# Optimization experiments

Hardware: AMD Instinct MI355X
Metric: run time of the kernel (lower is better)

Reference implementation:

```python
import jax, jax.numpy as jnp
import numpy as np

D_MODEL = 1024

def setup_inputs() -> dict:
    key = jax.random.key(0)
    ks = jax.random.split(key, 9)
    s = 1.0 / np.sqrt(D_MODEL)
    x = jax.random.normal(ks[0], (4, 2048, D_MODEL), dtype=jnp.float32)
    Wq = jax.random.uniform(ks[1], (D_MODEL, D_MODEL), jnp.float32, -s, s)
    bq = jax.random.uniform(ks[2], (D_MODEL,), jnp.float32, -s, s)
    Wk = jax.random.uniform(ks[3], (D_MODEL, D_MODEL), jnp.float32, -s, s)
    bk = jax.random.uniform(ks[4], (D_MODEL,), jnp.float32, -s, s)
    Wv = jax.random.uniform(ks[5], (D_MODEL, D_MODEL), jnp.float32, -s, s)
    bv = jax.random.uniform(ks[6], (D_MODEL,), jnp.float32, -s, s)
    Wo = jax.random.uniform(ks[7], (D_MODEL, D_MODEL), jnp.float32, -s, s)
    bo = jax.random.uniform(ks[8], (D_MODEL,), jnp.float32, -s, s)
    return {"x": x, "Wq": Wq, "bq": bq, "Wk": Wk, "bk": bk,
            "Wv": Wv, "bv": bv, "Wo": Wo, "bo": bo}

def reference(x, Wq, bq, Wk, bk, Wv, bv, Wo, bo):
    # Linear projections (weights stored as [in, out])
    q = x @ Wq + bq  # [b, s, d]
    k = x @ Wk + bk
    v = x @ Wv + bv
    d_k = q.shape[-1]
    scores = jnp.einsum("bqd,bkd->bqk", q, k) / jnp.sqrt(jnp.float32(d_k))
    p = jax.nn.softmax(scores, axis=-1)
    attn = jnp.einsum("bqk,bkd->bqd", p, v)
    return attn @ Wo + bo
```

## Files before the change

kernel.cpp:

```cpp
#include <hip/hip_runtime.h>
#include <stdint.h>

#define D_MODEL 1024
#define SEQ 2048
#define NBATCH 4

typedef __attribute__((ext_vector_type(4))) float f32x4;
typedef __attribute__((ext_vector_type(8))) __bf16 bf16x8;
typedef __attribute__((ext_vector_type(4))) unsigned short u16x4;

__device__ __forceinline__ float b2f(unsigned short u) {
    union { unsigned int i; float f; } c; c.i = ((unsigned int)u) << 16; return c.f;
}
__device__ __forceinline__ unsigned short f2b(float f) {
    union { float f; unsigned int i; } c; c.f = f;
    unsigned int u = c.i;
    u += 0x7FFFu + ((u >> 16) & 1u);
    return (unsigned short)(u >> 16);
}

__device__ __forceinline__ void glds16(void* lds, const void* g) {
    __builtin_amdgcn_global_load_lds((const __attribute__((address_space(1))) void*)g,
                                     (__attribute__((address_space(3))) void*)lds,
                                     16, 0, 0);
}

__device__ __forceinline__ void cfence() { asm volatile("" ::: "memory"); }

__device__ __forceinline__ void xcd_map(int& xx, int& yy, int& zz)
{
    const int gx = gridDim.x, gy = gridDim.y;
    int bid = blockIdx.x + gx * (blockIdx.y + gy * blockIdx.z);
    const int H = gy >> 3;
    const int xcd = bid & 7;
    int slot = bid >> 3;
    yy = xcd * H + (slot % H);
    slot /= H;
    xx = slot % gx;
    zz = slot / gx;
}

__device__ __forceinline__ void gemm_tile(const unsigned short* __restrict__ A,
                                          const unsigned short* __restrict__ Bt,
                                          int K, int m0, int n0,
                                          f32x4 (&acc)[4][4])
{
    __shared__ alignas(16) unsigned short As[3 * 128 * 32];
    __shared__ alignas(16) unsigned short Bs[3 * 128 * 32];

    const int t    = threadIdx.x;
    const int wave = t >> 6;
    const int lane = t & 63;

    const int srow = (wave << 4) + (lane >> 2);
    const int sch  = ((lane & 3) ^ ((srow >> 1) & 3)) * 8;

    const unsigned short* Ag = A  + (long)(m0 + srow) * K + sch;
    const unsigned short* Bg = Bt + (long)(n0 + srow) * K + sch;

    char* AsW = (char*)As + wave * 1024;
    char* BsW = (char*)Bs + wave * 1024;

    const int fr = lane & 15, quad = lane >> 4;
    const int wm = (wave >> 1) * 64, wn = (wave & 1) * 64;
    const int slot = (quad ^ ((fr >> 1) & 3)) * 16;
    const int aoff = (wm + fr) * 64 + slot;
    const int boff = (wn + fr) * 64 + slot;

    const int nt = K >> 5;

    auto stage = [&](int buf, int ko) {
        #pragma unroll
        for (int j = 0; j < 2; ++j) {
            glds16(AsW + buf * 8192 + j * 4096, Ag + (long)(j * 64) * K + ko);
            glds16(BsW + buf * 8192 + j * 4096, Bg + (long)(j * 64) * K + ko);
        }
    };

    stage(0, 0);
    stage(1, 32);
    asm volatile("s_waitcnt vmcnt(4)" ::: "memory");
    __builtin_amdgcn_sched_barrier(0);
    cfence(); __builtin_amdgcn_s_barrier(); cfence();

    int br = 0, bw = 2, ko = 64;
    for (int ti = 0; ti < nt; ++ti) {
        const char* Ab = (const char*)As + br * 8192;
        const char* Bb = (const char*)Bs + br * 8192;
        bf16x8 af[4], bv[4];
        #pragma unroll
        for (int i = 0; i < 4; ++i)
            af[i] = *(const bf16x8*)(Ab + aoff + i * 1024);
        #pragma unroll
        for (int i = 0; i < 4; ++i)
            bv[i] = *(const bf16x8*)(Bb + boff + i * 1024);

        const bool pf = (ti + 2 < nt);
        if (pf) { stage(bw, ko); ko += 32; }

        __builtin_amdgcn_s_setprio(1);
        #pragma unroll
        for (int mi = 0; mi < 4; ++mi)
            #pragma unroll
            for (int ni = 0; ni < 4; ++ni)
                acc[mi][ni] = __builtin_amdgcn_mfma_f32_16x16x32_bf16(
                                  af[mi], bv[ni], acc[mi][ni], 0, 0, 0);
        __builtin_amdgcn_s_setprio(0);

        if (pf)               asm volatile("s_waitcnt vmcnt(4)" ::: "memory");
        else if (ti + 1 < nt) asm volatile("s_waitcnt vmcnt(0)" ::: "memory");
        __builtin_amdgcn_sched_barrier(0);
        cfence(); __builtin_amdgcn_s_barrier(); cfence();

        br = (br == 2) ? 0 : br + 1;
        bw = (bw == 2) ? 0 : bw + 1;
    }
}

template<bool BIAS, typename OutT>
__global__ __launch_bounds__(256)
void gemm_bt(const unsigned short* __restrict__ A,
             const unsigned short* __restrict__ Bt,
             const float* __restrict__ bias,
             OutT* __restrict__ C,
             int N, int K, long sA, long sB, long sC)
{
    int xx, yy, zz;
    xcd_map(xx, yy, zz);
    A  += (long)zz * sA;
    Bt += (long)zz * sB;
    C  += (long)zz * sC;
    const int m0 = yy * 128;
    const int n0 = xx * 128;

    f32x4 acc[4][4] = {};
    gemm_tile(A, Bt, K, m0, n0, acc);

    const int t = threadIdx.x, wave = t >> 6, lane = t & 63;
    const int wm = (wave >> 1) * 64, wn = (wave & 1) * 64;
    const int fr = lane & 15, quad = lane >> 4;

    float bb[4] = {0.f, 0.f, 0.f, 0.f};
    if (BIAS) {
        #pragma unroll
        for (int ni = 0; ni < 4; ++ni)
            bb[ni] = bias[n0 + wn + ni * 16 + fr];
    }

    #pragma unroll
    for (int mi = 0; mi < 4; ++mi) {
        const int rowb = m0 + wm + mi * 16 + quad * 4;
        #pragma unroll
        for (int ni = 0; ni < 4; ++ni) {
            const int col = n0 + wn + ni * 16 + fr;
            f32x4 v = acc[mi][ni];
            if constexpr (sizeof(OutT) == 4) {
                #pragma unroll
                for (int r = 0; r < 4; ++r)
                    C[(long)(rowb + r) * N + col] = v[r] + bb[ni];
            } else {
                #pragma unroll
                for (int r = 0; r < 4; ++r)
                    C[(long)(rowb + r) * N + col] = (OutT)f2b(v[r] + bb[ni]);
            }
        }
    }
}

__global__ __launch_bounds__(256)
void qkv_gemm(const unsigned short* __restrict__ xb,
              const unsigned short* __restrict__ Wqt,
              const unsigned short* __restrict__ Wkt,
              const unsigned short* __restrict__ Wvt,
              const float* __restrict__ bq, const float* __restrict__ bk,
              const float* __restrict__ bv,
              unsigned short* __restrict__ Q, unsigned short* __restrict__ Kb,
              unsigned short* __restrict__ Vt)
{
    int xx, yy, zz;
    xcd_map(xx, yy, zz);

    const unsigned short* Bt; const float* bias; unsigned short* C; bool tstore = false;
    switch (zz) {
        case 0:  Bt = Wqt; bias = bq; C = Q;  break;
        case 1:  Bt = Wkt; bias = bk; C = Kb; break;
        default: Bt = Wvt; bias = bv; C = Vt; tstore = true; break;
    }
    const int m0 = yy * 128;
    const int n0 = xx * 128;
    const int N = D_MODEL, K = D_MODEL;

    f32x4 acc[4][4] = {};
    gemm_tile(xb, Bt, K, m0, n0, acc);

    const int t = threadIdx.x, wave = t >> 6, lane = t & 63;
    const int wm = (wave >> 1) * 64, wn = (wave & 1) * 64;
    const int fr = lane & 15, quad = lane >> 4;

    float bb[4];
    #pragma unroll
    for (int ni = 0; ni < 4; ++ni)
        bb[ni] = bias[n0 + wn + ni * 16 + fr];

    #pragma unroll
    for (int mi = 0; mi < 4; ++mi) {
        const int rowb = m0 + wm + mi * 16 + quad * 4;
        #pragma unroll
        for (int ni = 0; ni < 4; ++ni) {
            const int col = n0 + wn + ni * 16 + fr;
            f32x4 v = acc[mi][ni];
            if (!tstore) {
                #pragma unroll
                for (int r = 0; r < 4; ++r)
                    C[(long)(rowb + r) * N + col] = f2b(v[r] + bb[ni]);
            } else {
                u16x4 pk;
                #pragma unroll
                for (int r = 0; r < 4; ++r)
                    pk[r] = f2b(v[r] + bb[ni]);
                unsigned short* dst = C + ((long)(rowb >> 11)) * ((long)N * SEQ)
                                        + (long)col * SEQ + (rowb & (SEQ - 1));
                *(u16x4*)dst = pk;
            }
        }
    }
}

__global__ __launch_bounds__(256)
void softmax_inplace(unsigned short* __restrict__ S)
{
    const long row = blockIdx.x;
    unsigned short* s = S + row * SEQ;
    const int t = threadIdx.x;

    u16x4 a = ((const u16x4*)s)[t];
    u16x4 b = ((const u16x4*)s)[t + 256];
    float v[8];
    #pragma unroll
    for (int i = 0; i < 4; ++i) { v[i] = b2f(a[i]); v[4 + i] = b2f(b[i]); }

    float mx = v[0];
    #pragma unroll
    for (int i = 1; i < 8; ++i) mx = fmaxf(mx, v[i]);
    #pragma unroll
    for (int off = 32; off; off >>= 1) mx = fmaxf(mx, __shfl_xor(mx, off));

    __shared__ float red[8];
    const int wv = t >> 6, ln = t & 63;
    if (ln == 0) red[wv] = mx;
    __syncthreads();
    mx = fmaxf(fmaxf(red[0], red[1]), fmaxf(red[2], red[3]));

    const float sc = 0.03125f;
    float e[8], sum = 0.f;
    #pragma unroll
    for (int i = 0; i < 8; ++i) { e[i] = __expf((v[i] - mx) * sc); sum += e[i]; }
    #pragma unroll
    for (int off = 32; off; off >>= 1) sum += __shfl_xor(sum, off);
    if (ln == 0) red[4 + wv] = sum;
    __syncthreads();
    sum = (red[4] + red[5]) + (red[6] + red[7]);
    const float inv = 1.f / sum;

    u16x4 o;
    #pragma unroll
    for (int i = 0; i < 4; ++i) o[i] = f2b(e[i] * inv);
    ((u16x4*)s)[t] = o;
    #pragma unroll
    for (int i = 0; i < 4; ++i) o[i] = f2b(e[4 + i] * inv);
    ((u16x4*)s)[t + 256] = o;
}

__global__ __launch_bounds__(256)
void prep(const float* __restrict__ x, unsigned short* __restrict__ xb,
          const float* __restrict__ W0, const float* __restrict__ W1,
          const float* __restrict__ W2, const float* __restrict__ W3,
          unsigned short* __restrict__ T0, unsigned short* __restrict__ T1,
          unsigned short* __restrict__ T2, unsigned short* __restrict__ T3)
{
    const int bid = blockIdx.x;
    if (bid < 8192) {
        long i = ((long)bid * 256 + threadIdx.x) * 4;
        f32x4 v = *(const f32x4*)(x + i);
        u16x4 o;
        #pragma unroll
        for (int r = 0; r < 4; ++r) o[r] = f2b(v[r]);
        *(u16x4*)(xb + i) = o;
        return;
    }
    const int b2 = bid - 8192;
    const float* W; unsigned short* T;
    switch (b2 >> 10) {
        case 0:  W = W0; T = T0; break;
        case 1:  W = W1; T = T1; break;
        case 2:  W = W2; T = T2; break;
        default: W = W3; T = T3; break;
    }
    const int tile = b2 & 1023;
    const int bx = (tile & 31) * 32, by = (tile >> 5) * 32;
    __shared__ float buf[32][33];
    const int tx = threadIdx.x & 31, ty = threadIdx.x >> 5;
    #pragma unroll
    for (int i = 0; i < 32; i += 8)
        buf[ty + i][tx] = W[(long)(by + ty + i) * D_MODEL + bx + tx];
    __syncthreads();
    #pragma unroll
    for (int i = 0; i < 32; i += 8)
        T[(long)(bx + ty + i) * D_MODEL + by + tx] = f2b(buf[tx][ty + i]);
}

extern "C" void kernel_launch(void* const* d_in, const int* in_sizes, int n_in,
                              void* d_out, int out_size, void* d_ws, size_t ws_size,
                              hipStream_t stream)
{
    const float* x  = (const float*)d_in[0];
    const float* Wq = (const float*)d_in[1];
    const float* bq = (const float*)d_in[2];
    const float* Wk = (const float*)d_in[3];
    const float* bk = (const float*)d_in[4];
    const float* Wv = (const float*)d_in[5];
    const float* bv = (const float*)d_in[6];
    const float* Wo = (const float*)d_in[7];
    const float* bo = (const float*)d_in[8];
    float* out = (float*)d_out;

    char* ws = (char*)d_ws;
    const size_t MB = 1024ull * 1024ull;
    unsigned short* Wqt = (unsigned short*)(ws + 0 * MB);
    unsigned short* Wkt = (unsigned short*)(ws + 2 * MB);
    unsigned short* Wvt = (unsigned short*)(ws + 4 * MB);
    unsigned short* Wot = (unsigned short*)(ws + 6 * MB);
    unsigned short* xb  = (unsigned short*)(ws + 8 * MB);
    unsigned short* Q   = (unsigned short*)(ws + 24 * MB);
    unsigned short* Kb  = (unsigned short*)(ws + 40 * MB);
    unsigned short* Vt  = (unsigned short*)(ws + 56 * MB);
    unsigned short* At  = (unsigned short*)(ws + 72 * MB);
    unsigned short* S   = (unsigned short*)(ws + 88 * MB);

    const dim3 blk(256);

    prep<<<dim3(12288), blk, 0, stream>>>(x, xb, Wq, Wk, Wv, Wo, Wqt, Wkt, Wvt, Wot);

    qkv_gemm<<<dim3(8, 64, 3), blk, 0, stream>>>(xb, Wqt, Wkt, Wvt, bq, bk, bv, Q, Kb, Vt);

    gemm_bt<false, unsigned short><<<dim3(16, 16, 4), blk, 0, stream>>>(
        Q, Kb, nullptr, S, 2048, 1024,
        (long)2048 * 1024, (long)2048 * 1024, (long)2048 * 2048);

    softmax_inplace<<<dim3(NBATCH * SEQ), blk, 0, stream>>>(S);

    gemm_bt<false, unsigned short><<<dim3(8, 16, 4), blk, 0, stream>>>(
        S, Vt, nullptr, At, 1024, 2048,
        (long)2048 * 2048, (long)1024 * 2048, (long)2048 * 1024);

    gemm_bt<true, float><<<dim3(8, 64, 1), blk, 0, stream>>>(
        At, Wot, bo, out, 1024, 1024, 0, 0, 0);
}
```

Baseline: 294.6 us.

## Enlarge GEMM block tile to 256x128 with eight waves per block

All GEMM kernels move from 128x128 tiles with 4 waves to 256x128 tiles with 8 waves (512 threads). Each wave still computes a 64x64 sub-tile. The A staging now issues two row-halves per k-step and B one, with the LDS buffers and vmcnt waits resized to match. Grid sizes are halved along M. This doubles reuse of each loaded B tile and cuts total global traffic. In exchange there are fewer blocks: the PV and output GEMMs drop to 256 blocks, and LDS use per block grows to 72KB, which may hurt latency hiding.

New measurement: 278.2 us. -5.6%, faster.

```diff
diff --git a/kernel.cpp b/kernel.cpp
--- a/kernel.cpp
+++ b/kernel.cpp
@@ -45,7 +45,7 @@
                                           int K, int m0, int n0,
                                           f32x4 (&acc)[4][4])
 {
-    __shared__ alignas(16) unsigned short As[3 * 128 * 32];
+    __shared__ alignas(16) unsigned short As[3 * 256 * 32];
     __shared__ alignas(16) unsigned short Bs[3 * 128 * 32];
 
     const int t    = threadIdx.x;
@@ -62,30 +62,28 @@
     char* BsW = (char*)Bs + wave * 1024;
 
     const int fr = lane & 15, quad = lane >> 4;
-    const int wm = (wave >> 1) * 64, wn = (wave & 1) * 64;
+    const int wr = wave >> 1, wc = wave & 1;
     const int slot = (quad ^ ((fr >> 1) & 3)) * 16;
-    const int aoff = (wm + fr) * 64 + slot;
-    const int boff = (wn + fr) * 64 + slot;
+    const int aoff = (wr * 64 + fr) * 64 + slot;
+    const int boff = (wc * 64 + fr) * 64 + slot;
 
     const int nt = K >> 5;
 
     auto stage = [&](int buf, int ko) {
-        #pragma unroll
-        for (int j = 0; j < 2; ++j) {
-            glds16(AsW + buf * 8192 + j * 4096, Ag + (long)(j * 64) * K + ko);
-            glds16(BsW + buf * 8192 + j * 4096, Bg + (long)(j * 64) * K + ko);
-        }
+        glds16(AsW + buf * 16384,        Ag + ko);
+        glds16(AsW + buf * 16384 + 8192, Ag + (long)128 * K + ko);
+        glds16(BsW + buf * 8192,         Bg + ko);
     };
 
     stage(0, 0);
     stage(1, 32);
-    asm volatile("s_waitcnt vmcnt(4)" ::: "memory");
+    asm volatile("s_waitcnt vmcnt(3)" ::: "memory");
     __builtin_amdgcn_sched_barrier(0);
     cfence(); __builtin_amdgcn_s_barrier(); cfence();
 
     int br = 0, bw = 2, ko = 64;
     for (int ti = 0; ti < nt; ++ti) {
-        const char* Ab = (const char*)As + br * 8192;
+        const char* Ab = (const char*)As + br * 16384;
         const char* Bb = (const char*)Bs + br * 8192;
         bf16x8 af[4], bv[4];
         #pragma unroll
@@ -107,7 +105,7 @@
                                   af[mi], bv[ni], acc[mi][ni], 0, 0, 0);
         __builtin_amdgcn_s_setprio(0);
 
-        if (pf)               asm volatile("s_waitcnt vmcnt(4)" ::: "memory");
+        if (pf)               asm volatile("s_waitcnt vmcnt(3)" ::: "memory");
         else if (ti + 1 < nt) asm volatile("s_waitcnt vmcnt(0)" ::: "memory");
         __builtin_amdgcn_sched_barrier(0);
         cfence(); __builtin_amdgcn_s_barrier(); cfence();
@@ -118,7 +116,7 @@
 }
 
 template<bool BIAS, typename OutT>
-__global__ __launch_bounds__(256)
+__global__ __launch_bounds__(512)
 void gemm_bt(const unsigned short* __restrict__ A,
              const unsigned short* __restrict__ Bt,
              const float* __restrict__ bias,
@@ -130,29 +128,29 @@
     A  += (long)zz * sA;
     Bt += (long)zz * sB;
     C  += (long)zz * sC;
-    const int m0 = yy * 128;
+    const int m0 = yy * 256;
     const int n0 = xx * 128;
 
     f32x4 acc[4][4] = {};
     gemm_tile(A, Bt, K, m0, n0, acc);
 
     const int t = threadIdx.x, wave = t >> 6, lane = t & 63;
-    const int wm = (wave >> 1) * 64, wn = (wave & 1) * 64;
+    const int wr = wave >> 1, wc = wave & 1;
     const int fr = lane & 15, quad = lane >> 4;
 
     float bb[4] = {0.f, 0.f, 0.f, 0.f};
     if (BIAS) {
         #pragma unroll
         for (int ni = 0; ni < 4; ++ni)
-            bb[ni] = bias[n0 + wn + ni * 16 + fr];
+            bb[ni] = bias[n0 + wc * 64 + ni * 16 + fr];
     }
 
     #pragma unroll
     for (int mi = 0; mi < 4; ++mi) {
-        const int rowb = m0 + wm + mi * 16 + quad * 4;
+        const int rowb = m0 + wr * 64 + mi * 16 + quad * 4;
         #pragma unroll
         for (int ni = 0; ni < 4; ++ni) {
-            const int col = n0 + wn + ni * 16 + fr;
+            const int col = n0 + wc * 64 + ni * 16 + fr;
             f32x4 v = acc[mi][ni];
             if constexpr (sizeof(OutT) == 4) {
                 #pragma unroll
@@ -167,7 +165,7 @@
     }
 }
 
-__global__ __launch_bounds__(256)
+__global__ __launch_bounds__(512)
 void qkv_gemm(const unsigned short* __restrict__ xb,
               const unsigned short* __restrict__ Wqt,
               const unsigned short* __restrict__ Wkt,
@@ -186,7 +184,7 @@
         case 1:  Bt = Wkt; bias = bk; C = Kb; break;
         default: Bt = Wvt; bias = bv; C = Vt; tstore = true; break;
     }
-    const int m0 = yy * 128;
+    const int m0 = yy * 256;
     const int n0 = xx * 128;
     const int N = D_MODEL, K = D_MODEL;
 
@@ -194,20 +192,20 @@
     gemm_tile(xb, Bt, K, m0, n0, acc);
 
     const int t = threadIdx.x, wave = t >> 6, lane = t & 63;
-    const int wm = (wave >> 1) * 64, wn = (wave & 1) * 64;
+    const int wr = wave >> 1, wc = wave & 1;
     const int fr = lane & 15, quad = lane >> 4;
 
     float bb[4];
     #pragma unroll
     for (int ni = 0; ni < 4; ++ni)
-        bb[ni] = bias[n0 + wn + ni * 16 + fr];
+        bb[ni] = bias[n0 + wc * 64 + ni * 16 + fr];
 
     #pragma unroll
     for (int mi = 0; mi < 4; ++mi) {
-        const int rowb = m0 + wm + mi * 16 + quad * 4;
+        const int rowb = m0 + wr * 64 + mi * 16 + quad * 4;
         #pragma unroll
         for (int ni = 0; ni < 4; ++ni) {
-            const int col = n0 + wn + ni * 16 + fr;
+            const int col = n0 + wc * 64 + ni * 16 + fr;
             f32x4 v = acc[mi][ni];
             if (!tstore) {
                 #pragma unroll
@@ -337,22 +335,23 @@
     unsigned short* At  = (unsigned short*)(ws + 72 * MB);
     unsigned short* S   = (unsigned short*)(ws + 88 * MB);
 
-    const dim3 blk(256);
-
-    prep<<<dim3(12288), blk, 0, stream>>>(x, xb, Wq, Wk, Wv, Wo, Wqt, Wkt, Wvt, Wot);
-
-    qkv_gemm<<<dim3(8, 64, 3), blk, 0, stream>>>(xb, Wqt, Wkt, Wvt, bq, bk, bv, Q, Kb, Vt);
-
-    gemm_bt<false, unsigned short><<<dim3(16, 16, 4), blk, 0, stream>>>(
+    const dim3 blk256(256);
+    const dim3 blk512(512);
+
+    prep<<<dim3(12288), blk256, 0, stream>>>(x, xb, Wq, Wk, Wv, Wo, Wqt, Wkt, Wvt, Wot);
+
+    qkv_gemm<<<dim3(8, 32, 3), blk512, 0, stream>>>(xb, Wqt, Wkt, Wvt, bq, bk, bv, Q, Kb, Vt);
+
+    gemm_bt<false, unsigned short><<<dim3(16, 8, 4), blk512, 0, stream>>>(
         Q, Kb, nullptr, S, 2048, 1024,
         (long)2048 * 1024, (long)2048 * 1024, (long)2048 * 2048);
 
-    softmax_inplace<<<dim3(NBATCH * SEQ), blk, 0, stream>>>(S);
-
-    gemm_bt<false, unsigned short><<<dim3(8, 16, 4), blk, 0, stream>>>(
+    softmax_inplace<<<dim3(NBATCH * SEQ), blk256, 0, stream>>>(S);
+
+    gemm_bt<false, unsigned short><<<dim3(8, 8, 4), blk512, 0, stream>>>(
         S, Vt, nullptr, At, 1024, 2048,
         (long)2048 * 2048, (long)1024 * 2048, (long)2048 * 1024);
 
-    gemm_bt<true, float><<<dim3(8, 64, 1), blk, 0, stream>>>(
+    gemm_bt<true, float><<<dim3(8, 32, 1), blk512, 0, stream>>>(
         At, Wot, bo, out, 1024, 1024, 0, 0, 0);
 }
```

## Widen GEMM tiles to 128x256 with eight N-fragments per wave

Applied to the files above, without the earlier changes.

Doubles the N dimension of every GEMM block tile from 128 to 256, so each wave computes a 64x128 sub-tile with 32 accumulators instead of 16. B staging loads four 64-row slabs per K-step into a larger LDS buffer, and the grids are halved along x. This raises arithmetic intensity per LDS and global load, but it doubles accumulator register pressure (launch bounds now ask for 2 blocks per CU) and halves the number of blocks. Fewer blocks could underfill the CUs on the smaller launches, such as the 256-block attention-value GEMM.

New measurement: 296.0 us. No clear change (+0.5%).

```diff
diff --git a/kernel.cpp b/kernel.cpp
--- a/kernel.cpp
+++ b/kernel.cpp
@@ -43,10 +43,10 @@
 __device__ __forceinline__ void gemm_tile(const unsigned short* __restrict__ A,
                                           const unsigned short* __restrict__ Bt,
                                           int K, int m0, int n0,
-                                          f32x4 (&acc)[4][4])
+                                          f32x4 (&acc)[4][8])
 {
     __shared__ alignas(16) unsigned short As[3 * 128 * 32];
-    __shared__ alignas(16) unsigned short Bs[3 * 128 * 32];
+    __shared__ alignas(16) unsigned short Bs[3 * 256 * 32];
 
     const int t    = threadIdx.x;
     const int wave = t >> 6;
@@ -62,37 +62,39 @@
     char* BsW = (char*)Bs + wave * 1024;
 
     const int fr = lane & 15, quad = lane >> 4;
-    const int wm = (wave >> 1) * 64, wn = (wave & 1) * 64;
+    const int wr = wave >> 1, wc = wave & 1;
     const int slot = (quad ^ ((fr >> 1) & 3)) * 16;
-    const int aoff = (wm + fr) * 64 + slot;
-    const int boff = (wn + fr) * 64 + slot;
+    const int aoff = (wr * 64  + fr) * 64 + slot;
+    const int boff = (wc * 128 + fr) * 64 + slot;
 
     const int nt = K >> 5;
 
     auto stage = [&](int buf, int ko) {
-        #pragma unroll
-        for (int j = 0; j < 2; ++j) {
-            glds16(AsW + buf * 8192 + j * 4096, Ag + (long)(j * 64) * K + ko);
-            glds16(BsW + buf * 8192 + j * 4096, Bg + (long)(j * 64) * K + ko);
-        }
+        glds16(AsW + buf * 8192,         Ag + ko);
+        glds16(AsW + buf * 8192 + 4096,  Ag + (long)64 * K + ko);
+        glds16(BsW + buf * 16384,          Bg + ko);
+        glds16(BsW + buf * 16384 +  4096,  Bg + (long)64  * K + ko);
+        glds16(BsW + buf * 16384 +  8192,  Bg + (long)128 * K + ko);
+        glds16(BsW + buf * 16384 + 12288,  Bg + (long)192 * K + ko);
     };
 
     stage(0, 0);
     stage(1, 32);
-    asm volatile("s_waitcnt vmcnt(4)" ::: "memory");
+    asm volatile("s_waitcnt vmcnt(6)" ::: "memory");
     __builtin_amdgcn_sched_barrier(0);
     cfence(); __builtin_amdgcn_s_barrier(); cfence();
 
     int br = 0, bw = 2, ko = 64;
     for (int ti = 0; ti < nt; ++ti) {
         const char* Ab = (const char*)As + br * 8192;
-        const char* Bb = (const char*)Bs + br * 8192;
-        bf16x8 af[4], bv[4];
+        const char* Bb = (const char*)Bs + br * 16384;
+
+        bf16x8 af[4], bv[8];
         #pragma unroll
         for (int i = 0; i < 4; ++i)
             af[i] = *(const bf16x8*)(Ab + aoff + i * 1024);
         #pragma unroll
-        for (int i = 0; i < 4; ++i)
+        for (int i = 0; i < 8; ++i)
             bv[i] = *(const bf16x8*)(Bb + boff + i * 1024);
 
         const bool pf = (ti + 2 < nt);
@@ -102,12 +104,12 @@
         #pragma unroll
         for (int mi = 0; mi < 4; ++mi)
             #pragma unroll
-            for (int ni = 0; ni < 4; ++ni)
+            for (int ni = 0; ni < 8; ++ni)
                 acc[mi][ni] = __builtin_amdgcn_mfma_f32_16x16x32_bf16(
                                   af[mi], bv[ni], acc[mi][ni], 0, 0, 0);
         __builtin_amdgcn_s_setprio(0);
 
-        if (pf)               asm volatile("s_waitcnt vmcnt(4)" ::: "memory");
+        if (pf)               asm volatile("s_waitcnt vmcnt(6)" ::: "memory");
         else if (ti + 1 < nt) asm volatile("s_waitcnt vmcnt(0)" ::: "memory");
         __builtin_amdgcn_sched_barrier(0);
         cfence(); __builtin_amdgcn_s_barrier(); cfence();
@@ -118,7 +120,7 @@
 }
 
 template<bool BIAS, typename OutT>
-__global__ __launch_bounds__(256)
+__global__ __launch_bounds__(256, 2)
 void gemm_bt(const unsigned short* __restrict__ A,
              const unsigned short* __restrict__ Bt,
              const float* __restrict__ bias,
@@ -131,28 +133,28 @@
     Bt += (long)zz * sB;
     C  += (long)zz * sC;
     const int m0 = yy * 128;
-    const int n0 = xx * 128;
-
-    f32x4 acc[4][4] = {};
+    const int n0 = xx * 256;
+
+    f32x4 acc[4][8] = {};
     gemm_tile(A, Bt, K, m0, n0, acc);
 
     const int t = threadIdx.x, wave = t >> 6, lane = t & 63;
-    const int wm = (wave >> 1) * 64, wn = (wave & 1) * 64;
+    const int wr = wave >> 1, wc = wave & 1;
     const int fr = lane & 15, quad = lane >> 4;
 
-    float bb[4] = {0.f, 0.f, 0.f, 0.f};
+    float bb[8] = {};
     if (BIAS) {
         #pragma unroll
-        for (int ni = 0; ni < 4; ++ni)
-            bb[ni] = bias[n0 + wn + ni * 16 + fr];
+        for (int ni = 0; ni < 8; ++ni)
+            bb[ni] = bias[n0 + wc * 128 + ni * 16 + fr];
     }
 
     #pragma unroll
     for (int mi = 0; mi < 4; ++mi) {
-        const int rowb = m0 + wm + mi * 16 + quad * 4;
-        #pragma unroll
-        for (int ni = 0; ni < 4; ++ni) {
-            const int col = n0 + wn + ni * 16 + fr;
+        const int rowb = m0 + wr * 64 + mi * 16 + quad * 4;
+        #pragma unroll
+        for (int ni = 0; ni < 8; ++ni) {
+            const int col = n0 + wc * 128 + ni * 16 + fr;
             f32x4 v = acc[mi][ni];
             if constexpr (sizeof(OutT) == 4) {
                 #pragma unroll
@@ -167,7 +169,7 @@
     }
 }
 
-__global__ __launch_bounds__(256)
+__global__ __launch_bounds__(256, 2)
 void qkv_gemm(const unsigned short* __restrict__ xb,
               const unsigned short* __restrict__ Wqt,
               const unsigned short* __restrict__ Wkt,
@@ -187,27 +189,27 @@
         default: Bt = Wvt; bias = bv; C = Vt; tstore = true; break;
     }
     const int m0 = yy * 128;
-    const int n0 = xx * 128;
+    const int n0 = xx * 256;
     const int N = D_MODEL, K = D_MODEL;
 
-    f32x4 acc[4][4] = {};
+    f32x4 acc[4][8] = {};
     gemm_tile(xb, Bt, K, m0, n0, acc);
 
     const int t = threadIdx.x, wave = t >> 6, lane = t & 63;
-    const int wm = (wave >> 1) * 64, wn = (wave & 1) * 64;
+    const int wr = wave >> 1, wc = wave & 1;
     const int fr = lane & 15, quad = lane >> 4;
 
-    float bb[4];
-    #pragma unroll
-    for (int ni = 0; ni < 4; ++ni)
-        bb[ni] = bias[n0 + wn + ni * 16 + fr];
+    float bb[8];
+    #pragma unroll
+    for (int ni = 0; ni < 8; ++ni)
+        bb[ni] = bias[n0 + wc * 128 + ni * 16 + fr];
 
     #pragma unroll
     for (int mi = 0; mi < 4; ++mi) {
-        const int rowb = m0 + wm + mi * 16 + quad * 4;
-        #pragma unroll
-        for (int ni = 0; ni < 4; ++ni) {
-            const int col = n0 + wn + ni * 16 + fr;
+        const int rowb = m0 + wr * 64 + mi * 16 + quad * 4;
+        #pragma unroll
+        for (int ni = 0; ni < 8; ++ni) {
+            const int col = n0 + wc * 128 + ni * 16 + fr;
             f32x4 v = acc[mi][ni];
             if (!tstore) {
                 #pragma unroll
@@ -341,18 +343,18 @@
 
     prep<<<dim3(12288), blk, 0, stream>>>(x, xb, Wq, Wk, Wv, Wo, Wqt, Wkt, Wvt, Wot);
 
-    qkv_gemm<<<dim3(8, 64, 3), blk, 0, stream>>>(xb, Wqt, Wkt, Wvt, bq, bk, bv, Q, Kb, Vt);
-
-    gemm_bt<false, unsigned short><<<dim3(16, 16, 4), blk, 0, stream>>>(
+    qkv_gemm<<<dim3(4, 64, 3), blk, 0, stream>>>(xb, Wqt, Wkt, Wvt, bq, bk, bv, Q, Kb, Vt);
+
+    gemm_bt<false, unsigned short><<<dim3(8, 16, 4), blk, 0, stream>>>(
         Q, Kb, nullptr, S, 2048, 1024,
         (long)2048 * 1024, (long)2048 * 1024, (long)2048 * 2048);
 
     softmax_inplace<<<dim3(NBATCH * SEQ), blk, 0, stream>>>(S);
 
-    gemm_bt<false, unsigned short><<<dim3(8, 16, 4), blk, 0, stream>>>(
+    gemm_bt<false, unsigned short><<<dim3(4, 16, 4), blk, 0, stream>>>(
         S, Vt, nullptr, At, 1024, 2048,
         (long)2048 * 2048, (long)1024 * 2048, (long)2048 * 1024);
 
-    gemm_bt<true, float><<<dim3(8, 64, 1), blk, 0, stream>>>(
+    gemm_bt<true, float><<<dim3(4, 64, 1), blk, 0, stream>>>(
         At, Wot, bo, out, 1024, 1024, 0, 0, 0);
 }
```
